# Performance work log

Measured on AMD Instinct MI355X. Metric: run time of the kernel, lower is better.

Reference implementation:

```python
import jax, jax.numpy as jnp
import numpy as np

N = 32768
DEG = 9        # 8 neighbors + self-loop
B = 8
K = 3          # Chebyshev degree
IN_CH = 8
OUT_CH = 2
HID = 64


def setup_inputs() -> dict:
    key = jax.random.key(0)
    ks = jax.random.split(key, 14)
    # structured 9-neighbor stencil (CSR-like sorted rows), honoring graph sparsity
    offs = np.arange(-4, 5)
    rows_np = np.repeat(np.arange(N), DEG).astype(np.int32)
    cols_np = ((rows_np.reshape(N, DEG) + offs[None, :]) % N).reshape(-1).astype(np.int32)
    vals = jax.random.normal(ks[0], (N * DEG,), jnp.float32) * 0.1
    x = jax.random.normal(ks[1], (B, N, IN_CH), jnp.float32)

    def w(k, fin, fout):
        return jax.random.normal(k, (K * fin, fout), jnp.float32) * 0.05

    def b(k, fout):
        return jax.random.normal(k, (fout,), jnp.float32) * 0.01

    return dict(
        x=x, rows=jnp.asarray(rows_np), cols=jnp.asarray(cols_np), vals=vals,
        W1=w(ks[2], IN_CH, HID), b1=b(ks[3], HID),
        W2=w(ks[4], HID, HID), b2=b(ks[5], HID),
        W3=w(ks[6], HID, HID), b3=b(ks[7], HID),
        W4=w(ks[8], HID, HID), b4=b(ks[9], HID),
        W5=w(ks[10], HID, OUT_CH), b5=b(ks[11], OUT_CH),
    )


def _spmm(rows, cols, vals, x):
    # sparse Laplacian @ x ; x: [B, N, C] -> [B, N, C]
    g = x[:, cols, :] * vals[None, :, None]          # [B, nnz, C]
    g = jnp.swapaxes(g, 0, 1)                        # [nnz, B, C]
    y = jax.ops.segment_sum(g, rows, num_segments=N) # [N, B, C]
    return jnp.swapaxes(y, 0, 1)


def _cheb_conv(rows, cols, vals, x, W, b):
    # Chebyshev recursion: T0 = x, T1 = L x, Tk = 2 L T_{k-1} - T_{k-2}
    x0 = x
    xs = [x0]
    if K > 1:
        x1 = _spmm(rows, cols, vals, x0)
        xs.append(x1)
        for _ in range(K - 2):
            x2 = 2.0 * _spmm(rows, cols, vals, x1) - x0
            xs.append(x2)
            x0, x1 = x1, x2
    xk = jnp.concatenate(xs, axis=-1)                # [B, N, K*Fin]
    return jnp.einsum('bnf,fo->bno', xk, W) + b


def reference(x, rows, cols, vals, W1, b1, W2, b2, W3, b3, W4, b4, W5, b5):
    h = jax.nn.elu(_cheb_conv(rows, cols, vals, x, W1, b1))
    h = jax.nn.elu(_cheb_conv(rows, cols, vals, h, W2, b2))
    h = jax.nn.elu(_cheb_conv(rows, cols, vals, h, W3, b3))
    h = jax.nn.elu(_cheb_conv(rows, cols, vals, h, W4, b4))
    out = _cheb_conv(rows, cols, vals, h, W5, b5)    # no ELU on last layer
    return out
```

## Files before the change

kernel.cpp:

```cpp
#include <hip/hip_runtime.h>
#include <math.h>

#define N_PIX 32768
#define DEG 9
#define BATCH 8
#define TILE 64

typedef unsigned short u16;
typedef __attribute__((ext_vector_type(8))) short bf16x8;
typedef __attribute__((ext_vector_type(16))) float f32x16;

__device__ __forceinline__ u16 bf16_rn(float x) {
    unsigned int u = __builtin_bit_cast(unsigned int, x);
    u += 0x7fffu + ((u >> 16) & 1u);
    return (u16)(u >> 16);
}
__device__ __forceinline__ float bf16_to_f(u16 u) {
    unsigned int v = ((unsigned int)u) << 16;
    return __builtin_bit_cast(float, v);
}


__global__ void prep_all(const float* __restrict__ W1, const float* __restrict__ W2,
                         const float* __restrict__ W3, const float* __restrict__ W4,
                         const float* __restrict__ vals,
                         u16* __restrict__ out, float* __restrict__ vpre) {
    if (blockIdx.x < 3) {
        const float* W = (blockIdx.x == 0) ? W2 : (blockIdx.x == 1) ? W3 : W4;
        u16* o = out + (size_t)blockIdx.x * 24576;
        const int base = blockIdx.y * 768;
        for (int idx = base + threadIdx.x; idx < base + 768; idx += 256) {
            int j = idx & 7;
            int lane = (idx >> 3) & 63;
            int rest = idx >> 9;
            int s = rest & 3, tt = rest >> 2;
            int mt = tt & 1, mat = tt >> 1;
            int k = s * 16 + (lane >> 5) * 8 + j;
            int m = mt * 32 + (lane & 31);
            float x = (mat == 0) ? W[k * 64 + m] - W[(128 + k) * 64 + m]
                    : (mat == 1) ? W[(64 + k) * 64 + m]
                                 : W[(128 + k) * 64 + m];
            u16 hi = bf16_rn(x);
            o[idx] = hi;
            o[12288 + idx] = bf16_rn(x - bf16_to_f(hi));
        }
    } else if (blockIdx.x == 3) {
        u16* o = out + 73728;
        const int base = blockIdx.y * 1536;
        for (int e = base + threadIdx.x; e < base + 1536 && e < 24576; e += 256) {
            int j = e & 7;
            int lane = (e >> 3) & 63;
            int tt = e >> 12;
            int mt = tt & 1, mat = tt >> 1;
            int m = mt * 32 + (lane & 31);
            float x = 0.f;
            if ((lane >> 5) == 0) {
                x = (mat == 0) ? W1[j * 64 + m] - W1[(16 + j) * 64 + m]
                  : (mat == 1) ? W1[(8 + j) * 64 + m]
                               : W1[(16 + j) * 64 + m];
            }
            u16 hi = bf16_rn(x);
            o[e] = hi;
            o[24576 + e] = bf16_rn(x - bf16_to_f(hi));
        }
    } else if (blockIdx.x >= 5) {
        const int vb = (blockIdx.x - 5) * 16 + blockIdx.y;
        const int base = vb * 3072;
        #pragma unroll
        for (int k = 0; k < 12; ++k) {
            int idx = base + k * 256 + threadIdx.x;
            int g = idx / 12, j = idx - g * 12;
            vpre[idx] = (j < 9) ? vals[(size_t)g * 9 + j] : 0.f;
        }
    }
}

template<bool FIRST>
__global__ __launch_bounds__(512, 6)
void cheb_conv(const float* __restrict__ Xf, const u16* __restrict__ Xh,
               const u16* __restrict__ Xl, const float* __restrict__ Vpre,
               const u16* __restrict__ wt, int wbase, const float* __restrict__ bias,
               u16* __restrict__ Yh, u16* __restrict__ Yl) {
    constexpr int LD = 68;
    __shared__ alignas(16) float P2s[80 * LD];
    __shared__ alignas(16) float P1s[72 * LD];
    __shared__ alignas(16) float Vs[72 * 12];

    const int tid = threadIdx.x;
    const int bx = ((blockIdx.x & 7) << 6) | (blockIdx.x >> 3);
    const int n0 = bx * TILE;
    const int b  = blockIdx.y;
    const size_t bplane = (size_t)b * ((size_t)N_PIX * 64);

    if (tid < 216) {
        int r = tid / 3, q = tid - r * 3;
        int g = (n0 - 4 + r) & (N_PIX - 1);
        *(float4*)&Vs[r * 12 + q * 4] = *(const float4*)&Vpre[(size_t)g * 12 + q * 4];
    }

    const int w = tid >> 6, lane = tid & 63;
    const int half = lane >> 5, m31 = lane & 31;

    auto gemm_accs = [&](int mat, int rowoff, int rl, f32x16& acc0, f32x16& acc1) {
        const int g = (n0 + rowoff + rl) & (N_PIX - 1);
        constexpr int SC   = FIRST ? 1 : 4;
        constexpr int LOFF = FIRST ? 24576 : 12288;
        const u16* a0p = wt + wbase + lane * 8 + (FIRST ? (mat * 2) * 4096 : mat * 4096);
        const u16* a1p = a0p + (FIRST ? 4096 : 2048);
        const size_t bbase = bplane + (size_t)(g >> 5) * 2048 + (size_t)(g & 31) * 8;
        const float* xfp = FIRST ? (Xf + (size_t)b * N_PIX * 8 + (size_t)g * 8) : nullptr;
        #pragma unroll
        for (int s = 0; s < SC; ++s) {
            bf16x8 bh = {}, bl = {};
            if constexpr (FIRST) {
                if (half == 0) {
                    float xv[8];
                    *(float4*)&xv[0] = *(const float4*)&xfp[0];
                    *(float4*)&xv[4] = *(const float4*)&xfp[4];
                    #pragma unroll
                    for (int e = 0; e < 8; ++e) {
                        u16 hh = bf16_rn(xv[e]);
                        bh[e] = (short)hh;
                        bl[e] = (short)bf16_rn(xv[e] - bf16_to_f(hh));
                    }
                }
            } else {
                const size_t off = bbase + (size_t)(s * 2 + half) * 256;
                bh = *(const bf16x8*)&Xh[off];
                bl = *(const bf16x8*)&Xl[off];
            }
            bf16x8 a0h = *(const bf16x8*)(a0p + s * 512);
            bf16x8 a0l = *(const bf16x8*)(a0p + s * 512 + LOFF);
            bf16x8 a1h = *(const bf16x8*)(a1p + s * 512);
            bf16x8 a1l = *(const bf16x8*)(a1p + s * 512 + LOFF);
            acc0 = __builtin_amdgcn_mfma_f32_32x32x16_bf16(a0l, bh, acc0, 0, 0, 0);
            acc0 = __builtin_amdgcn_mfma_f32_32x32x16_bf16(a0h, bl, acc0, 0, 0, 0);
            acc0 = __builtin_amdgcn_mfma_f32_32x32x16_bf16(a0h, bh, acc0, 0, 0, 0);
            acc1 = __builtin_amdgcn_mfma_f32_32x32x16_bf16(a1l, bh, acc1, 0, 0, 0);
            acc1 = __builtin_amdgcn_mfma_f32_32x32x16_bf16(a1h, bl, acc1, 0, 0, 0);
            acc1 = __builtin_amdgcn_mfma_f32_32x32x16_bf16(a1h, bh, acc1, 0, 0, 0);
        }
    };
    auto scatter = [&](float* dst, int rl, const f32x16& a0, const f32x16& a1) {
        #pragma unroll
        for (int q = 0; q < 4; ++q) {
            float4 v0 = {a0[4 * q], a0[4 * q + 1], a0[4 * q + 2], a0[4 * q + 3]};
            float4 v1 = {a1[4 * q], a1[4 * q + 1], a1[4 * q + 2], a1[4 * q + 3]};
            *(float4*)&dst[rl * LD + q * 8 + half * 4]      = v0;
            *(float4*)&dst[rl * LD + 32 + q * 8 + half * 4] = v1;
        }
    };

    if (w < 6) {
        int mat, ntile, rowoff; float* dst;
        if (w < 3) { mat = 2; ntile = (w == 0) ? 0 : ((w == 1) ? 32 : 48); rowoff = -8; dst = P2s; }
        else       { mat = 1; ntile = (w == 3) ? 0 : ((w == 4) ? 32 : 40); rowoff = -4; dst = P1s; }
        f32x16 acc0 = {}, acc1 = {};
        gemm_accs(mat, rowoff, ntile + m31, acc0, acc1);
        scatter(dst, ntile + m31, acc0, acc1);
    }
    __syncthreads();

    f32x16 pacc0 = {}, pacc1 = {};
    int prl = 0;
    if (tid < 384) {
        const int st = tid >> 4, c0 = (tid & 15) << 2;
        const int r0 = st * 3;
        float4 win[11];
        #pragma unroll
        for (int l = 0; l < 11; ++l)
            win[l] = *(const float4*)&P2s[(r0 + l) * LD + c0];
        #pragma unroll
        for (int r = 0; r < 3; ++r) {
            const int sg = r0 + r;
            float4 vA = *(const float4*)&Vs[sg * 12];
            float4 vB = *(const float4*)&Vs[sg * 12 + 4];
            float v8 = Vs[sg * 12 + 8];
            const float vj[9] = {vA.x, vA.y, vA.z, vA.w, vB.x, vB.y, vB.z, vB.w, v8};
            float4 a = {0.f, 0.f, 0.f, 0.f};
            #pragma unroll
            for (int j = 0; j < 9; ++j) {
                float4 xv = win[r + j];
                a.x = fmaf(vj[j], xv.x, a.x); a.y = fmaf(vj[j], xv.y, a.y);
                a.z = fmaf(vj[j], xv.z, a.z); a.w = fmaf(vj[j], xv.w, a.w);
            }
            float4 p1 = *(const float4*)&P1s[sg * LD + c0];
            p1.x = fmaf(2.f, a.x, p1.x); p1.y = fmaf(2.f, a.y, p1.y);
            p1.z = fmaf(2.f, a.z, p1.z); p1.w = fmaf(2.f, a.w, p1.w);
            *(float4*)&P1s[sg * LD + c0] = p1;
        }
    } else {
        prl = ((w == 6) ? 0 : 32) + m31;
        gemm_accs(0, 0, prl, pacc0, pacc1);
    }
    __syncthreads();

    if (tid >= 384) scatter(P2s, prl, pacc0, pacc1);
    __syncthreads();

    {
        const int est = tid >> 4, ecx = tid & 15;
        const int ey0 = est * 2, ec0 = ecx << 2;
        float4 win[10];
        #pragma unroll
        for (int l = 0; l < 10; ++l)
            win[l] = *(const float4*)&P1s[(ey0 + l) * LD + ec0];
        const float4 bb = *(const float4*)&bias[ec0];
        #pragma unroll
        for (int r = 0; r < 2; ++r) {
            const int y = ey0 + r;
            float4 vA = *(const float4*)&Vs[(y + 4) * 12];
            float4 vB = *(const float4*)&Vs[(y + 4) * 12 + 4];
            float v8 = Vs[(y + 4) * 12 + 8];
            const float vj[9] = {vA.x, vA.y, vA.z, vA.w, vB.x, vB.y, vB.z, vB.w, v8};
            float4 a = bb;
            #pragma unroll
            for (int j = 0; j < 9; ++j) {
                float4 xv = win[r + j];
                a.x = fmaf(vj[j], xv.x, a.x); a.y = fmaf(vj[j], xv.y, a.y);
                a.z = fmaf(vj[j], xv.z, a.z); a.w = fmaf(vj[j], xv.w, a.w);
            }
            float4 p0 = *(const float4*)&P2s[y * LD + ec0];
            float yv[4] = {a.x + p0.x, a.y + p0.y, a.z + p0.z, a.w + p0.w};
            ushort4 h, l;
            u16 hh;
            #pragma unroll
            for (int e = 0; e < 4; ++e)
                yv[e] = yv[e] > 0.f ? yv[e] : __expf(yv[e]) - 1.f;
            hh = bf16_rn(yv[0]); h.x = hh; l.x = bf16_rn(yv[0] - bf16_to_f(hh));
            hh = bf16_rn(yv[1]); h.y = hh; l.y = bf16_rn(yv[1] - bf16_to_f(hh));
            hh = bf16_rn(yv[2]); h.z = hh; l.z = bf16_rn(yv[2] - bf16_to_f(hh));
            hh = bf16_rn(yv[3]); h.w = hh; l.w = bf16_rn(yv[3] - bf16_to_f(hh));
            const int gy = n0 + y;
            size_t dsto = bplane + (size_t)(gy >> 5) * 2048 + (size_t)(ecx >> 1) * 256
                        + (size_t)(gy & 31) * 8 + (size_t)(ecx & 1) * 4;
            *(ushort4*)&Yh[dsto] = h;
            *(ushort4*)&Yl[dsto] = l;
        }
    }
}

__global__ __launch_bounds__(512, 4)
void cheb_last4(const u16* __restrict__ Xh, const u16* __restrict__ Xl,
                const float* __restrict__ vals,
                const float* __restrict__ W5, const float* __restrict__ b5,
                float* __restrict__ Y) {
    __shared__ alignas(16) float Pb[144 * 8];
    __shared__ alignas(16) float Sb[136 * 2];
    __shared__ alignas(16) float Vs[136 * 12];

    const int tid = threadIdx.x;
    const int n0 = blockIdx.x * 128;
    const int b  = blockIdx.y;
    const size_t bplane = (size_t)b * ((size_t)N_PIX * 64);

    for (int i = tid; i < 1224; i += 512) {
        int sr = i / 9, j = i - sr * 9;
        int g = (n0 - 4 + sr) & (N_PIX - 1);
        Vs[sr * 12 + j] = vals[(size_t)g * DEG + j];
    }

    {
        const int w = tid >> 6, lane = tid & 63;
        const int half = lane >> 5, m31 = lane & 31;
        if (w < 5) {
            const int ntile = (w == 4) ? 112 : w * 32;
            const int rl = ntile + m31;
            const int g = (n0 - 8 + rl) & (N_PIX - 1);
            const size_t bbase = bplane + (size_t)(g >> 5) * 2048 + (g & 31) * 8;
            const bool valid = m31 < 6;
            const int seg = m31 >> 1, o = m31 & 1;
            f32x16 acc = {};
            #pragma unroll
            for (int s = 0; s < 4; ++s) {
                const size_t off = bbase + (size_t)(s * 2 + half) * 256;
                bf16x8 bh = *(const bf16x8*)&Xh[off];
                bf16x8 bl = *(const bf16x8*)&Xl[off];
                bf16x8 ah, al;
                #pragma unroll
                for (int j = 0; j < 8; ++j) {
                    int k = s * 16 + half * 8 + j;
                    float x = valid ? W5[(seg * 64 + k) * 2 + o] : 0.f;
                    u16 hh = bf16_rn(x);
                    ah[j] = (short)hh;
                    al[j] = (short)bf16_rn(x - bf16_to_f(hh));
                }
                acc = __builtin_amdgcn_mfma_f32_32x32x16_bf16(al, bh, acc, 0, 0, 0);
                acc = __builtin_amdgcn_mfma_f32_32x32x16_bf16(ah, bl, acc, 0, 0, 0);
                acc = __builtin_amdgcn_mfma_f32_32x32x16_bf16(ah, bh, acc, 0, 0, 0);
            }
            if (half == 0) {
                float4 v = {acc[0], acc[1], acc[2], acc[3]};
                *(float4*)&Pb[rl * 8] = v;
            } else {
                Pb[rl * 8 + 4] = acc[0];
                Pb[rl * 8 + 5] = acc[1];
            }
        }
    }
    __syncthreads();

    if (tid < 272) {
        const int sg = tid >> 1, o = tid & 1;
        float q = 0.f;
        #pragma unroll
        for (int j = 0; j < DEG; ++j)
            q = fmaf(Vs[sg * 12 + j], Pb[(sg + j) * 8 + 4 + o], q);
        Sb[sg * 2 + o] = Pb[(sg + 4) * 8 + 2 + o] + 2.f * q;
    }
    __syncthreads();

    if (tid < 256) {
        const int y = tid >> 1, o = tid & 1;
        float q = 0.f;
        #pragma unroll
        for (int j = 0; j < DEG; ++j)
            q = fmaf(Vs[(y + 4) * 12 + j], Sb[(y + j) * 2 + o], q);
        float v = Pb[(y + 8) * 8 + o] - Pb[(y + 8) * 8 + 4 + o] + q + b5[o];
        Y[((size_t)b * N_PIX + n0 + y) * 2 + o] = v;
    }
}

extern "C" void kernel_launch(void* const* d_in, const int* in_sizes, int n_in,
                              void* d_out, int out_size, void* d_ws, size_t ws_size,
                              hipStream_t stream) {
    const float* x    = (const float*)d_in[0];
    const float* vals = (const float*)d_in[3];
    const float* W1 = (const float*)d_in[4];
    const float* b1 = (const float*)d_in[5];
    const float* W2 = (const float*)d_in[6];
    const float* b2 = (const float*)d_in[7];
    const float* W3 = (const float*)d_in[8];
    const float* b3 = (const float*)d_in[9];
    const float* W4 = (const float*)d_in[10];
    const float* b4 = (const float*)d_in[11];
    const float* W5 = (const float*)d_in[12];
    const float* b5 = (const float*)d_in[13];
    float* out = (float*)d_out;

    const size_t PL = (size_t)BATCH * N_PIX * 64;
    u16* Ah_g = (u16*)d_ws;
    u16* Al_g = Ah_g + PL;
    u16* Bh_g = Ah_g + 2 * PL;
    u16* Bl_g = Ah_g + 3 * PL;
    u16* wt = (u16*)d_out;
    float* vpre = (float*)((char*)d_out + 262144);

    dim3 grid(N_PIX / TILE, BATCH);
    prep_all<<<dim3(13, 16), dim3(256), 0, stream>>>(W1, W2, W3, W4, vals, wt, vpre);
    cheb_conv<true><<<grid, dim3(512), 0, stream>>>(x, nullptr, nullptr, vpre, wt, 73728, b1, Ah_g, Al_g);
    cheb_conv<false><<<grid, dim3(512), 0, stream>>>(nullptr, Ah_g, Al_g, vpre, wt, 0,     b2, Bh_g, Bl_g);
    cheb_conv<false><<<grid, dim3(512), 0, stream>>>(nullptr, Bh_g, Bl_g, vpre, wt, 24576, b3, Ah_g, Al_g);
    cheb_conv<false><<<grid, dim3(512), 0, stream>>>(nullptr, Ah_g, Al_g, vpre, wt, 49152, b4, Bh_g, Bl_g);
    cheb_last4<<<dim3(N_PIX / 128, BATCH), dim3(512), 0, stream>>>(Bh_g, Bl_g, vals, W5, b5, out);
}
```

Measured before the change: 293.6 us.

## Swizzle LDS tiles, drop Vs staging, raise occupancy to eight waves

Replaces the padded LDS row stride (68) with a 64-wide layout that rotates column indices per row to avoid bank conflicts. It removes the shared Vs buffer and reads the Laplacian values directly from global memory. Launch bounds rise from 6 to 8 waves per SIMD. Together these shrink LDS use so more blocks can be resident, at the cost of repeated global or cache reads of vals and tighter register limits that may cause spills.

```diff
diff --git a/kernel.cpp b/kernel.cpp
--- a/kernel.cpp
+++ b/kernel.cpp
@@ -18,6 +18,10 @@
 __device__ __forceinline__ float bf16_to_f(u16 u) {
     unsigned int v = ((unsigned int)u) << 16;
     return __builtin_bit_cast(float, v);
+}
+
+__device__ __forceinline__ int rot(int row, int c) {
+    return row * 64 + ((c + ((row & 7) << 3)) & 63);
 }
 
 
@@ -76,27 +80,19 @@
 }
 
 template<bool FIRST>
-__global__ __launch_bounds__(512, 6)
+__global__ __launch_bounds__(512, 8)
 void cheb_conv(const float* __restrict__ Xf, const u16* __restrict__ Xh,
                const u16* __restrict__ Xl, const float* __restrict__ Vpre,
                const u16* __restrict__ wt, int wbase, const float* __restrict__ bias,
                u16* __restrict__ Yh, u16* __restrict__ Yl) {
-    constexpr int LD = 68;
-    __shared__ alignas(16) float P2s[80 * LD];
-    __shared__ alignas(16) float P1s[72 * LD];
-    __shared__ alignas(16) float Vs[72 * 12];
+    __shared__ alignas(16) float P2s[80 * 64];
+    __shared__ alignas(16) float P1s[72 * 64];
 
     const int tid = threadIdx.x;
     const int bx = ((blockIdx.x & 7) << 6) | (blockIdx.x >> 3);
     const int n0 = bx * TILE;
     const int b  = blockIdx.y;
     const size_t bplane = (size_t)b * ((size_t)N_PIX * 64);
-
-    if (tid < 216) {
-        int r = tid / 3, q = tid - r * 3;
-        int g = (n0 - 4 + r) & (N_PIX - 1);
-        *(float4*)&Vs[r * 12 + q * 4] = *(const float4*)&Vpre[(size_t)g * 12 + q * 4];
-    }
 
     const int w = tid >> 6, lane = tid & 63;
     const int half = lane >> 5, m31 = lane & 31;
@@ -146,8 +142,8 @@
         for (int q = 0; q < 4; ++q) {
             float4 v0 = {a0[4 * q], a0[4 * q + 1], a0[4 * q + 2], a0[4 * q + 3]};
             float4 v1 = {a1[4 * q], a1[4 * q + 1], a1[4 * q + 2], a1[4 * q + 3]};
-            *(float4*)&dst[rl * LD + q * 8 + half * 4]      = v0;
-            *(float4*)&dst[rl * LD + 32 + q * 8 + half * 4] = v1;
+            *(float4*)&dst[rot(rl, q * 8 + half * 4)]      = v0;
+            *(float4*)&dst[rot(rl, 32 + q * 8 + half * 4)] = v1;
         }
     };
 
@@ -169,13 +165,14 @@
         float4 win[11];
         #pragma unroll
         for (int l = 0; l < 11; ++l)
-            win[l] = *(const float4*)&P2s[(r0 + l) * LD + c0];
+            win[l] = *(const float4*)&P2s[rot(r0 + l, c0)];
         #pragma unroll
         for (int r = 0; r < 3; ++r) {
             const int sg = r0 + r;
-            float4 vA = *(const float4*)&Vs[sg * 12];
-            float4 vB = *(const float4*)&Vs[sg * 12 + 4];
-            float v8 = Vs[sg * 12 + 8];
+            const float* vp = &Vpre[(size_t)((n0 - 4 + sg) & (N_PIX - 1)) * 12];
+            float4 vA = *(const float4*)vp;
+            float4 vB = *(const float4*)(vp + 4);
+            float v8 = vp[8];
             const float vj[9] = {vA.x, vA.y, vA.z, vA.w, vB.x, vB.y, vB.z, vB.w, v8};
             float4 a = {0.f, 0.f, 0.f, 0.f};
             #pragma unroll
@@ -184,10 +181,10 @@
                 a.x = fmaf(vj[j], xv.x, a.x); a.y = fmaf(vj[j], xv.y, a.y);
                 a.z = fmaf(vj[j], xv.z, a.z); a.w = fmaf(vj[j], xv.w, a.w);
             }
-            float4 p1 = *(const float4*)&P1s[sg * LD + c0];
+            float4 p1 = *(const float4*)&P1s[rot(sg, c0)];
             p1.x = fmaf(2.f, a.x, p1.x); p1.y = fmaf(2.f, a.y, p1.y);
             p1.z = fmaf(2.f, a.z, p1.z); p1.w = fmaf(2.f, a.w, p1.w);
-            *(float4*)&P1s[sg * LD + c0] = p1;
+            *(float4*)&P1s[rot(sg, c0)] = p1;
         }
     } else {
         prl = ((w == 6) ? 0 : 32) + m31;
@@ -204,14 +201,15 @@
         float4 win[10];
         #pragma unroll
         for (int l = 0; l < 10; ++l)
-            win[l] = *(const float4*)&P1s[(ey0 + l) * LD + ec0];
+            win[l] = *(const float4*)&P1s[rot(ey0 + l, ec0)];
         const float4 bb = *(const float4*)&bias[ec0];
         #pragma unroll
         for (int r = 0; r < 2; ++r) {
             const int y = ey0 + r;
-            float4 vA = *(const float4*)&Vs[(y + 4) * 12];
-            float4 vB = *(const float4*)&Vs[(y + 4) * 12 + 4];
-            float v8 = Vs[(y + 4) * 12 + 8];
+            const float* vp = &Vpre[(size_t)((n0 + y) & (N_PIX - 1)) * 12];
+            float4 vA = *(const float4*)vp;
+            float4 vB = *(const float4*)(vp + 4);
+            float v8 = vp[8];
             const float vj[9] = {vA.x, vA.y, vA.z, vA.w, vB.x, vB.y, vB.z, vB.w, v8};
             float4 a = bb;
             #pragma unroll
@@ -220,7 +218,7 @@
                 a.x = fmaf(vj[j], xv.x, a.x); a.y = fmaf(vj[j], xv.y, a.y);
                 a.z = fmaf(vj[j], xv.z, a.z); a.w = fmaf(vj[j], xv.w, a.w);
             }
-            float4 p0 = *(const float4*)&P2s[y * LD + ec0];
+            float4 p0 = *(const float4*)&P2s[rot(y, ec0)];
             float yv[4] = {a.x + p0.x, a.y + p0.y, a.z + p0.z, a.w + p0.w};
             ushort4 h, l;
             u16 hh;
```

Result: slower. 303.9 us (+3.5%).
